# Kernel tuning notes

Hardware: AMD Instinct MI355X
Metric: run time of the kernel (lower is better)

## Reference

```python
import jax, jax.numpy as jnp
import numpy as np

N_NODES = 50000
N_EDGES = 800000
IN_DIM = 128
OUT_DIM = 64
LEAKY_SLOPE = 0.01  # torch F.leaky_relu default


def setup_inputs() -> dict:
    key = jax.random.key(0)
    k1, k2, k3, k4, k5 = jax.random.split(key, 5)
    features = jax.random.normal(k1, (N_NODES, IN_DIM), dtype=jnp.float32)
    src = jax.random.randint(k2, (N_EDGES,), 0, N_NODES, dtype=jnp.int32)
    dst = jax.random.randint(k3, (N_EDGES,), 0, N_NODES, dtype=jnp.int32)
    # fc: Linear(in_dim, out_dim, bias=False) -> stored as [in_dim, out_dim]
    W_fc = jax.random.normal(k4, (IN_DIM, OUT_DIM), dtype=jnp.float32) * (1.0 / np.sqrt(IN_DIM))
    # attn_fc: Linear(2*out_dim, 1, bias=False) -> stored as flat [2*out_dim]
    a_vec = jax.random.normal(k5, (2 * OUT_DIM,), dtype=jnp.float32) * (1.0 / np.sqrt(2 * OUT_DIM))
    return {"features": features, "src": src, "dst": dst, "W_fc": W_fc, "a_vec": a_vec}


def reference(features, src, dst, W_fc, a_vec):
    n = features.shape[0]
    d = W_fc.shape[1]
    # node projection: z = fc(features)
    z = features @ W_fc                                   # [N, d]
    # attn score: a^T [z_src || z_dst] = (z @ a_src)[src] + (z @ a_dst)[dst]
    az_src = z @ a_vec[:d]                                # [N]
    az_dst = z @ a_vec[d:]                                # [N]
    e = jax.nn.leaky_relu(az_src[src] + az_dst[dst], negative_slope=LEAKY_SLOPE)  # [E]
    # segment softmax over edges grouped by destination node
    e_max = jax.ops.segment_max(e, dst, num_segments=n)   # [N] (-inf for isolated nodes)
    e_exp = jnp.exp(e - e_max[dst])                       # [E]
    e_sum = jax.ops.segment_sum(e_exp, dst, num_segments=n)  # [N]
    alpha = e_exp / e_sum[dst]                            # [E]
    # weighted scatter-sum of source features to destination nodes
    h = jax.ops.segment_sum(alpha[:, None] * z[src], dst, num_segments=n)  # [N, d]
    return h
```

## Files before the change

### kernel.cpp

```cpp
#include <hip/hip_runtime.h>
#include <hip/hip_bf16.h>
#include <math.h>

#define N_NODES 50000
#define N_EDGES 800000
#define IN_DIM  128
#define OUT_DIM 64
#define LEAKY   0.01f

#define PROJ_ROWS 64
#define PROJ_NB   ((N_NODES + PROJ_ROWS - 1) / PROJ_ROWS)
#define EDGE_NB   ((N_EDGES + 255) / 256)

#define SCAN_B   1024
#define SCAN_NB  ((N_NODES + SCAN_B - 1) / SCAN_B)

typedef float vfloat2 __attribute__((ext_vector_type(2)));

__global__ __launch_bounds__(256) void proj_hist_kernel(
        const float* __restrict__ feat, const float* __restrict__ W,
        const float* __restrict__ a,
        __hip_bfloat16* __restrict__ zb,
        float* __restrict__ az_src, float* __restrict__ az_dst,
        const int* __restrict__ dst, int* __restrict__ counts,
        int* __restrict__ rank) {
    __shared__ float fs[PROJ_ROWS * IN_DIM];
    int tid = threadIdx.x;

    if (blockIdx.x >= PROJ_NB) {
        int i = (blockIdx.x - PROJ_NB) * 256 + tid;
        if (i < N_EDGES) rank[i] = atomicAdd(&counts[dst[i]], 1);
        return;
    }

    int row0 = blockIdx.x * PROJ_ROWS;
    int nrows = N_NODES - row0; if (nrows > PROJ_ROWS) nrows = PROJ_ROWS;

    const float4* gsrc = (const float4*)(feat + (size_t)row0 * IN_DIM);
    if (nrows == PROJ_ROWS) {
#pragma unroll
        for (int i = 0; i < 8; ++i) {
            int idx = tid + i * 256;
            ((float4*)fs)[idx] = gsrc[idx];
        }
    } else {
        int lim = nrows * (IN_DIM / 4);
#pragma unroll
        for (int i = 0; i < 8; ++i) {
            int idx = tid + i * 256;
            if (idx < lim) ((float4*)fs)[idx] = gsrc[idx];
        }
    }
    __syncthreads();

    int lane  = tid & 63;
    int wv    = tid >> 6;
    int cg    = lane & 15;
    int rg    = lane >> 4;
    int rbase = wv * 16 + rg * 4;

    float acc[4][4];
#pragma unroll
    for (int r = 0; r < 4; ++r)
#pragma unroll
        for (int c = 0; c < 4; ++c) acc[r][c] = 0.f;

    const float* fr0 = &fs[rbase * IN_DIM];
    for (int kk = 0; kk < IN_DIM / 4; ++kk) {
        int kr = (kk + rg) & 31;
        float4 w0 = *(const float4*)&W[(kr * 4 + 0) * OUT_DIM + cg * 4];
        float4 w1 = *(const float4*)&W[(kr * 4 + 1) * OUT_DIM + cg * 4];
        float4 w2 = *(const float4*)&W[(kr * 4 + 2) * OUT_DIM + cg * 4];
        float4 w3 = *(const float4*)&W[(kr * 4 + 3) * OUT_DIM + cg * 4];
#pragma unroll
        for (int r = 0; r < 4; ++r) {
            float4 f = *(const float4*)&fr0[r * IN_DIM + kr * 4];
            acc[r][0] = fmaf(f.x, w0.x, acc[r][0]);
            acc[r][1] = fmaf(f.x, w0.y, acc[r][1]);
            acc[r][2] = fmaf(f.x, w0.z, acc[r][2]);
            acc[r][3] = fmaf(f.x, w0.w, acc[r][3]);
            acc[r][0] = fmaf(f.y, w1.x, acc[r][0]);
            acc[r][1] = fmaf(f.y, w1.y, acc[r][1]);
            acc[r][2] = fmaf(f.y, w1.z, acc[r][2]);
            acc[r][3] = fmaf(f.y, w1.w, acc[r][3]);
            acc[r][0] = fmaf(f.z, w2.x, acc[r][0]);
            acc[r][1] = fmaf(f.z, w2.y, acc[r][1]);
            acc[r][2] = fmaf(f.z, w2.z, acc[r][2]);
            acc[r][3] = fmaf(f.z, w2.w, acc[r][3]);
            acc[r][0] = fmaf(f.w, w3.x, acc[r][0]);
            acc[r][1] = fmaf(f.w, w3.y, acc[r][1]);
            acc[r][2] = fmaf(f.w, w3.z, acc[r][2]);
            acc[r][3] = fmaf(f.w, w3.w, acc[r][3]);
        }
    }

    float4 a1 = *(const float4*)&a[cg * 4];
    float4 a2 = *(const float4*)&a[OUT_DIM + cg * 4];
#pragma unroll
    for (int r = 0; r < 4; ++r) {
        int row = row0 + rbase + r;
        if (row < N_NODES) {
            __hip_bfloat16 z0 = __float2bfloat16(acc[r][0]);
            __hip_bfloat16 z1 = __float2bfloat16(acc[r][1]);
            __hip_bfloat16 z2 = __float2bfloat16(acc[r][2]);
            __hip_bfloat16 z3 = __float2bfloat16(acc[r][3]);
            ushort4 zp;
            zp.x = *(unsigned short*)&z0;
            zp.y = *(unsigned short*)&z1;
            zp.z = *(unsigned short*)&z2;
            zp.w = *(unsigned short*)&z3;
            *(ushort4*)&zb[(size_t)row * OUT_DIM + cg * 4] = zp;

            float s1 = acc[r][0] * a1.x + acc[r][1] * a1.y +
                       acc[r][2] * a1.z + acc[r][3] * a1.w;
            float s2 = acc[r][0] * a2.x + acc[r][1] * a2.y +
                       acc[r][2] * a2.z + acc[r][3] * a2.w;
#pragma unroll
            for (int off = 1; off < 16; off <<= 1) {
                s1 += __shfl_xor(s1, off, 64);
                s2 += __shfl_xor(s2, off, 64);
            }
            if (cg == 0) { az_src[row] = s1; az_dst[row] = s2; }
        }
    }
}

__global__ __launch_bounds__(SCAN_B) void scan1_kernel(
        const int* __restrict__ counts, int* __restrict__ offsets,
        int* __restrict__ blocksums) {
    __shared__ int s[SCAN_B];
    int i = blockIdx.x * SCAN_B + threadIdx.x;
    int v = (i < N_NODES) ? counts[i] : 0;
    s[threadIdx.x] = v;
    __syncthreads();
    for (int off = 1; off < SCAN_B; off <<= 1) {
        int t = (threadIdx.x >= off) ? s[threadIdx.x - off] : 0;
        __syncthreads();
        s[threadIdx.x] += t;
        __syncthreads();
    }
    if (i < N_NODES) offsets[i] = s[threadIdx.x] - v;
    if (threadIdx.x == SCAN_B - 1) blocksums[blockIdx.x] = s[SCAN_B - 1];
}

__global__ __launch_bounds__(SCAN_B) void scan3_kernel(
        int* __restrict__ offsets, const int* __restrict__ blocksums) {
    __shared__ int bs[64];
    if (threadIdx.x < 64) {
        int lane = threadIdx.x;
        int v = (lane < SCAN_NB) ? blocksums[lane] : 0;
        int inc = v;
#pragma unroll
        for (int off = 1; off < 64; off <<= 1) {
            int t = __shfl_up(inc, off, 64);
            if (lane >= off) inc += t;
        }
        bs[lane] = inc - v;
    }
    __syncthreads();
    int i = blockIdx.x * SCAN_B + threadIdx.x;
    if (i < N_NODES) offsets[i] += bs[blockIdx.x];
    if (i == 0) offsets[N_NODES] = N_EDGES;
}

__global__ __launch_bounds__(256) void build_csr_kernel(
        const int* __restrict__ src, const int* __restrict__ dst,
        const int* __restrict__ rank, const int* __restrict__ offsets,
        const float* __restrict__ az_src, vfloat2* __restrict__ edge_rec) {
    int i = blockIdx.x * 256 + threadIdx.x;
    if (i >= N_EDGES) return;
    int t = dst[i];
    int s = src[i];
    int pos = offsets[t] + rank[i];
    vfloat2 rec;
    rec.x = __int_as_float(s);
    rec.y = az_src[s];
    __builtin_nontemporal_store(rec, &edge_rec[pos]);
}

__global__ __launch_bounds__(256) void node_fused_kernel(
        const int* __restrict__ offsets, const vfloat2* __restrict__ edge_rec,
        const float* __restrict__ az_dst,
        const __hip_bfloat16* __restrict__ zb, float* __restrict__ h) {
    int lane = threadIdx.x & 63;
    int w    = threadIdx.x >> 6;
    int t    = blockIdx.x * 4 + w;
    if (t >= N_NODES) return;
    int beg = offsets[t];
    int end = offsets[t + 1];
    float az_d = az_dst[t];

    float acc0 = 0.f, acc1 = 0.f, acc2 = 0.f, acc3 = 0.f;
    float ss0 = 0.f, ss1 = 0.f, ss2 = 0.f, ss3 = 0.f;
    int i = beg;
    for (; i + 4 <= end; i += 4) {
        vfloat2 r0 = edge_rec[i];
        vfloat2 r1 = edge_rec[i + 1];
        vfloat2 r2 = edge_rec[i + 2];
        vfloat2 r3 = edge_rec[i + 3];
        float v0 = r0.y + az_d;
        float v1 = r1.y + az_d;
        float v2 = r2.y + az_d;
        float v3 = r3.y + az_d;
        v0 = v0 > 0.f ? v0 : LEAKY * v0;
        v1 = v1 > 0.f ? v1 : LEAKY * v1;
        v2 = v2 > 0.f ? v2 : LEAKY * v2;
        v3 = v3 > 0.f ? v3 : LEAKY * v3;
        float x0 = __expf(v0), x1 = __expf(v1);
        float x2 = __expf(v2), x3 = __expf(v3);
        ss0 += x0; ss1 += x1; ss2 += x2; ss3 += x3;
        int s0 = __float_as_int(r0.x);
        int s1 = __float_as_int(r1.x);
        int s2 = __float_as_int(r2.x);
        int s3 = __float_as_int(r3.x);
        acc0 = fmaf(x0, __bfloat162float(zb[(size_t)s0 * OUT_DIM + lane]), acc0);
        acc1 = fmaf(x1, __bfloat162float(zb[(size_t)s1 * OUT_DIM + lane]), acc1);
        acc2 = fmaf(x2, __bfloat162float(zb[(size_t)s2 * OUT_DIM + lane]), acc2);
        acc3 = fmaf(x3, __bfloat162float(zb[(size_t)s3 * OUT_DIM + lane]), acc3);
    }
    for (; i < end; ++i) {
        vfloat2 r0 = edge_rec[i];
        float v0 = r0.y + az_d;
        v0 = v0 > 0.f ? v0 : LEAKY * v0;
        float x0 = __expf(v0);
        ss0 += x0;
        int s0 = __float_as_int(r0.x);
        acc0 = fmaf(x0, __bfloat162float(zb[(size_t)s0 * OUT_DIM + lane]), acc0);
    }
    float ssum = (ss0 + ss1) + (ss2 + ss3);
    float inv  = (end > beg) ? 1.f / ssum : 0.f;
    h[(size_t)t * OUT_DIM + lane] = ((acc0 + acc1) + (acc2 + acc3)) * inv;
}

extern "C" void kernel_launch(void* const* d_in, const int* in_sizes, int n_in,
                              void* d_out, int out_size, void* d_ws, size_t ws_size,
                              hipStream_t stream) {
    const float* feat = (const float*)d_in[0];
    const int*   src  = (const int*)  d_in[1];
    const int*   dst  = (const int*)  d_in[2];
    const float* W    = (const float*)d_in[3];
    const float* a    = (const float*)d_in[4];
    float* h = (float*)d_out;

    vfloat2* edge_rec = (vfloat2*)d_ws;
    float*  az_src    = (float*)(edge_rec + N_EDGES);
    float*  az_dst    = az_src + N_NODES;
    int*    counts    = (int*)(az_dst + N_NODES);
    int*    offsets   = counts + N_NODES;
    int*    blocksums = offsets + N_NODES + 1;
    int*    rank      = blocksums + 64;
    __hip_bfloat16* zb = (__hip_bfloat16*)(rank + N_EDGES);

    (void)hipMemsetAsync(counts, 0, sizeof(int) * N_NODES, stream);

    proj_hist_kernel<<<PROJ_NB + EDGE_NB, 256, 0, stream>>>(
        feat, W, a, zb, az_src, az_dst, dst, counts, rank);

    scan1_kernel<<<SCAN_NB, SCAN_B, 0, stream>>>(counts, offsets, blocksums);
    scan3_kernel<<<SCAN_NB, SCAN_B, 0, stream>>>(offsets, blocksums);

    build_csr_kernel<<<EDGE_NB, 256, 0, stream>>>(src, dst, rank, offsets,
                                                  az_src, edge_rec);

    node_fused_kernel<<<(N_NODES + 3) / 4, 256, 0, stream>>>(
        offsets, edge_rec, az_dst, zb, h);
}
```

Measured before the change: 191.4 us.

## Fold block-prefix scan pass into consumers and unroll gather loop to 8

Removes the separate scan3 kernel launch. The build_csr and node kernels now each recompute the 64-entry block prefix of blocksums in shared memory and add it to the local offsets on the fly. The node aggregation loop is also unrolled from 4 to 8 edges with more independent accumulators, giving more gathers in flight. The cost is a wave-level shuffle scan plus a __syncthreads in every block of both kernels, and higher register use in the node kernel.

```diff
diff --git a/kernel.cpp b/kernel.cpp
--- a/kernel.cpp
+++ b/kernel.cpp
@@ -143,9 +143,8 @@
     if (threadIdx.x == SCAN_B - 1) blocksums[blockIdx.x] = s[SCAN_B - 1];
 }
 
-__global__ __launch_bounds__(SCAN_B) void scan3_kernel(
-        int* __restrict__ offsets, const int* __restrict__ blocksums) {
-    __shared__ int bs[64];
+__device__ __forceinline__ void load_block_prefix(
+        const int* __restrict__ blocksums, int* bs) {
     if (threadIdx.x < 64) {
         int lane = threadIdx.x;
         int v = (lane < SCAN_NB) ? blocksums[lane] : 0;
@@ -158,20 +157,20 @@
         bs[lane] = inc - v;
     }
     __syncthreads();
-    int i = blockIdx.x * SCAN_B + threadIdx.x;
-    if (i < N_NODES) offsets[i] += bs[blockIdx.x];
-    if (i == 0) offsets[N_NODES] = N_EDGES;
 }
 
 __global__ __launch_bounds__(256) void build_csr_kernel(
         const int* __restrict__ src, const int* __restrict__ dst,
         const int* __restrict__ rank, const int* __restrict__ offsets,
+        const int* __restrict__ blocksums,
         const float* __restrict__ az_src, vfloat2* __restrict__ edge_rec) {
+    __shared__ int bs[64];
+    load_block_prefix(blocksums, bs);
     int i = blockIdx.x * 256 + threadIdx.x;
     if (i >= N_EDGES) return;
     int t = dst[i];
     int s = src[i];
-    int pos = offsets[t] + rank[i];
+    int pos = offsets[t] + bs[t >> 10] + rank[i];
     vfloat2 rec;
     rec.x = __int_as_float(s);
     rec.y = az_src[s];
@@ -179,57 +178,78 @@
 }
 
 __global__ __launch_bounds__(256) void node_fused_kernel(
-        const int* __restrict__ offsets, const vfloat2* __restrict__ edge_rec,
+        const int* __restrict__ offsets, const int* __restrict__ blocksums,
+        const vfloat2* __restrict__ edge_rec,
         const float* __restrict__ az_dst,
         const __hip_bfloat16* __restrict__ zb, float* __restrict__ h) {
+    __shared__ int bs[64];
+    load_block_prefix(blocksums, bs);
     int lane = threadIdx.x & 63;
     int w    = threadIdx.x >> 6;
     int t    = blockIdx.x * 4 + w;
     if (t >= N_NODES) return;
-    int beg = offsets[t];
-    int end = offsets[t + 1];
+    int beg = offsets[t] + bs[t >> 10];
+    int end = (t + 1 < N_NODES) ? offsets[t + 1] + bs[(t + 1) >> 10] : N_EDGES;
     float az_d = az_dst[t];
 
-    float acc0 = 0.f, acc1 = 0.f, acc2 = 0.f, acc3 = 0.f;
-    float ss0 = 0.f, ss1 = 0.f, ss2 = 0.f, ss3 = 0.f;
-    int i = beg;
-    for (; i + 4 <= end; i += 4) {
-        vfloat2 r0 = edge_rec[i];
-        vfloat2 r1 = edge_rec[i + 1];
-        vfloat2 r2 = edge_rec[i + 2];
-        vfloat2 r3 = edge_rec[i + 3];
-        float v0 = r0.y + az_d;
-        float v1 = r1.y + az_d;
-        float v2 = r2.y + az_d;
-        float v3 = r3.y + az_d;
+    float ac0 = 0.f, ac1 = 0.f, ac2 = 0.f, ac3 = 0.f;
+    float ac4 = 0.f, ac5 = 0.f, ac6 = 0.f, ac7 = 0.f;
+    float sm0 = 0.f, sm1 = 0.f, sm2 = 0.f, sm3 = 0.f;
+    float sm4 = 0.f, sm5 = 0.f, sm6 = 0.f, sm7 = 0.f;
+    int k = beg;
+    for (; k + 8 <= end; k += 8) {
+        vfloat2 r0 = edge_rec[k];
+        vfloat2 r1 = edge_rec[k + 1];
+        vfloat2 r2 = edge_rec[k + 2];
+        vfloat2 r3 = edge_rec[k + 3];
+        vfloat2 r4 = edge_rec[k + 4];
+        vfloat2 r5 = edge_rec[k + 5];
+        vfloat2 r6 = edge_rec[k + 6];
+        vfloat2 r7 = edge_rec[k + 7];
+        float v0 = r0.y + az_d, v1 = r1.y + az_d;
+        float v2 = r2.y + az_d, v3 = r3.y + az_d;
+        float v4 = r4.y + az_d, v5 = r5.y + az_d;
+        float v6 = r6.y + az_d, v7 = r7.y + az_d;
         v0 = v0 > 0.f ? v0 : LEAKY * v0;
         v1 = v1 > 0.f ? v1 : LEAKY * v1;
         v2 = v2 > 0.f ? v2 : LEAKY * v2;
         v3 = v3 > 0.f ? v3 : LEAKY * v3;
+        v4 = v4 > 0.f ? v4 : LEAKY * v4;
+        v5 = v5 > 0.f ? v5 : LEAKY * v5;
+        v6 = v6 > 0.f ? v6 : LEAKY * v6;
+        v7 = v7 > 0.f ? v7 : LEAKY * v7;
         float x0 = __expf(v0), x1 = __expf(v1);
         float x2 = __expf(v2), x3 = __expf(v3);
-        ss0 += x0; ss1 += x1; ss2 += x2; ss3 += x3;
-        int s0 = __float_as_int(r0.x);
-        int s1 = __float_as_int(r1.x);
-        int s2 = __float_as_int(r2.x);
-        int s3 = __float_as_int(r3.x);
-        acc0 = fmaf(x0, __bfloat162float(zb[(size_t)s0 * OUT_DIM + lane]), acc0);
-        acc1 = fmaf(x1, __bfloat162float(zb[(size_t)s1 * OUT_DIM + lane]), acc1);
-        acc2 = fmaf(x2, __bfloat162float(zb[(size_t)s2 * OUT_DIM + lane]), acc2);
-        acc3 = fmaf(x3, __bfloat162float(zb[(size_t)s3 * OUT_DIM + lane]), acc3);
-    }
-    for (; i < end; ++i) {
-        vfloat2 r0 = edge_rec[i];
+        float x4 = __expf(v4), x5 = __expf(v5);
+        float x6 = __expf(v6), x7 = __expf(v7);
+        sm0 += x0; sm1 += x1; sm2 += x2; sm3 += x3;
+        sm4 += x4; sm5 += x5; sm6 += x6; sm7 += x7;
+        int s0 = __float_as_int(r0.x), s1 = __float_as_int(r1.x);
+        int s2 = __float_as_int(r2.x), s3 = __float_as_int(r3.x);
+        int s4 = __float_as_int(r4.x), s5 = __float_as_int(r5.x);
+        int s6 = __float_as_int(r6.x), s7 = __float_as_int(r7.x);
+        ac0 = fmaf(x0, __bfloat162float(zb[(size_t)s0 * OUT_DIM + lane]), ac0);
+        ac1 = fmaf(x1, __bfloat162float(zb[(size_t)s1 * OUT_DIM + lane]), ac1);
+        ac2 = fmaf(x2, __bfloat162float(zb[(size_t)s2 * OUT_DIM + lane]), ac2);
+        ac3 = fmaf(x3, __bfloat162float(zb[(size_t)s3 * OUT_DIM + lane]), ac3);
+        ac4 = fmaf(x4, __bfloat162float(zb[(size_t)s4 * OUT_DIM + lane]), ac4);
+        ac5 = fmaf(x5, __bfloat162float(zb[(size_t)s5 * OUT_DIM + lane]), ac5);
+        ac6 = fmaf(x6, __bfloat162float(zb[(size_t)s6 * OUT_DIM + lane]), ac6);
+        ac7 = fmaf(x7, __bfloat162float(zb[(size_t)s7 * OUT_DIM + lane]), ac7);
+    }
+    for (; k < end; ++k) {
+        vfloat2 r0 = edge_rec[k];
         float v0 = r0.y + az_d;
         v0 = v0 > 0.f ? v0 : LEAKY * v0;
         float x0 = __expf(v0);
-        ss0 += x0;
+        sm0 += x0;
         int s0 = __float_as_int(r0.x);
-        acc0 = fmaf(x0, __bfloat162float(zb[(size_t)s0 * OUT_DIM + lane]), acc0);
-    }
-    float ssum = (ss0 + ss1) + (ss2 + ss3);
+        ac0 = fmaf(x0, __bfloat162float(zb[(size_t)s0 * OUT_DIM + lane]), ac0);
+    }
+    float ssum = ((sm0 + sm1) + (sm2 + sm3)) + ((sm4 + sm5) + (sm6 + sm7));
     float inv  = (end > beg) ? 1.f / ssum : 0.f;
-    h[(size_t)t * OUT_DIM + lane] = ((acc0 + acc1) + (acc2 + acc3)) * inv;
+    float hv   = ((ac0 + ac1) + (ac2 + ac3)) + ((ac4 + ac5) + (ac6 + ac7));
+    h[(size_t)t * OUT_DIM + lane] = hv * inv;
 }
 
 extern "C" void kernel_launch(void* const* d_in, const int* in_sizes, int n_in,
@@ -247,7 +267,7 @@
     float*  az_dst    = az_src + N_NODES;
     int*    counts    = (int*)(az_dst + N_NODES);
     int*    offsets   = counts + N_NODES;
-    int*    blocksums = offsets + N_NODES + 1;
+    int*    blocksums = offsets + N_NODES;
     int*    rank      = blocksums + 64;
     __hip_bfloat16* zb = (__hip_bfloat16*)(rank + N_EDGES);
 
@@ -257,11 +277,10 @@
         feat, W, a, zb, az_src, az_dst, dst, counts, rank);
 
     scan1_kernel<<<SCAN_NB, SCAN_B, 0, stream>>>(counts, offsets, blocksums);
-    scan3_kernel<<<SCAN_NB, SCAN_B, 0, stream>>>(offsets, blocksums);
 
     build_csr_kernel<<<EDGE_NB, 256, 0, stream>>>(src, dst, rank, offsets,
-                                                  az_src, edge_rec);
+                                                  blocksums, az_src, edge_rec);
 
     node_fused_kernel<<<(N_NODES + 3) / 4, 256, 0, stream>>>(
-        offsets, edge_rec, az_dst, zb, h);
-}
+        offsets, blocksums, edge_rec, az_dst, zb, h);
+}
```

After: 193.9 us. Within noise of the previous version (+1.3%).
